# Performance work log

Hardware: AMD Instinct MI355X
Metric: run time of the kernel (lower is better)

Reference implementation:

```python
import jax, jax.numpy as jnp
import numpy as np

B, T, D = 4, 2048, 512
H, HS = 8, 64            # n_head, head_size
E, K = 8, 2              # num_experts, top_k
CAP = int(B * T * K / E * 1.0)  # expert capacity = 2048
EPS = 1e-5


def setup_inputs() -> dict:
    key = jax.random.key(0)
    ks = jax.random.split(key, 16)
    s = lambda k, shp, fan: jax.random.normal(k, shp, jnp.float32) * (fan ** -0.5)
    return {
        "x": jax.random.normal(ks[0], (B, T, D), jnp.float32),
        "ln1_g": jnp.ones((D,), jnp.float32), "ln1_b": jnp.zeros((D,), jnp.float32),
        "Wq": s(ks[1], (H, D, HS), D), "Wk": s(ks[2], (H, D, HS), D), "Wv": s(ks[3], (H, D, HS), D),
        "Wo": s(ks[4], (D, D), D), "bo": jnp.zeros((D,), jnp.float32),
        "ln2_g": jnp.ones((D,), jnp.float32), "ln2_b": jnp.zeros((D,), jnp.float32),
        "Wg": s(ks[5], (D, E), D), "bg": jnp.zeros((E,), jnp.float32),
        "Wn": s(ks[6], (D, E), D), "bn": jnp.zeros((E,), jnp.float32),
        "W1": s(ks[7], (E, D, 4 * D), D), "b1": jnp.zeros((E, 4 * D), jnp.float32),
        "W2": s(ks[8], (E, 4 * D, D), 4 * D), "b2": jnp.zeros((E, D), jnp.float32),
    }


def _ln(x, g, b):
    m = jnp.mean(x, -1, keepdims=True)
    v = jnp.var(x, -1, keepdims=True)
    return (x - m) * jax.lax.rsqrt(v + EPS) * g + b


def _attn(h, Wq, Wk, Wv, Wo, bo):
    q = jnp.einsum('btd,hde->bhte', h, Wq)
    k = jnp.einsum('btd,hde->bhte', h, Wk)
    v = jnp.einsum('btd,hde->bhte', h, Wv)
    # NOTE: source scales by C**-0.5 with C = n_embed (not head_size)
    wei = jnp.einsum('bhte,bhse->bhts', q, k) * (D ** -0.5)
    causal = jnp.tril(jnp.ones((T, T), bool))
    wei = jnp.where(causal, wei, -jnp.inf)
    wei = jax.nn.softmax(wei, axis=-1)
    out = jnp.einsum('bhts,bhse->bhte', wei, v)              # [B,H,T,HS]
    out = out.transpose(0, 2, 1, 3).reshape(B, T, D)          # concat heads
    return out @ Wo + bo


def _moe(h, Wg, bg, Wn, bn, W1, b1, W2, b2):
    logits = h @ Wg + bg
    noise_logits = h @ Wn + bn
    noise = jax.random.normal(jax.random.key(42), logits.shape, logits.dtype) * jax.nn.softplus(noise_logits)
    noisy = logits + noise
    vals, idx = jax.lax.top_k(noisy, K)                       # [B,T,K]
    # softmax over -inf-masked sparse logits == softmax over top-k values, scattered
    gates = (jax.nn.softmax(vals, -1)[..., None] * jax.nn.one_hot(idx, E, dtype=h.dtype)).sum(-2)  # [B,T,E]
    flat_x = h.reshape(-1, D)
    flat_g = gates.reshape(-1, E)
    flat_idx = idx.reshape(-1, K)
    N = flat_x.shape[0]
    mask = (flat_idx[None] == jnp.arange(E)[:, None, None]).any(-1)   # [E,N]
    rank = jnp.cumsum(mask, axis=1) - 1
    keep = mask & (rank < CAP)                                 # first CAP tokens per expert
    slot = jnp.where(keep, rank, CAP)
    tok = jnp.arange(N, dtype=jnp.int32)

    def build(s, kp):
        buf = jnp.zeros(CAP + 1, jnp.int32).at[s].set(tok)
        vb = jnp.zeros(CAP + 1, bool).at[s].set(kp)
        return buf[:CAP], vb[:CAP]

    idx_buf, valid = jax.vmap(build)(slot, keep)               # [E,CAP]
    xg = flat_x[idx_buf]                                       # [E,CAP,D]
    mid = jax.nn.relu(jnp.einsum('ecd,edf->ecf', xg, W1) + b1[:, None, :])
    out = jnp.einsum('ecf,efd->ecd', mid, W2) + b2[:, None, :]
    gate_sel = flat_g[idx_buf, jnp.arange(E)[:, None]]         # [E,CAP]
    w = out * (gate_sel * valid.astype(h.dtype))[..., None]
    upd = jnp.zeros_like(flat_x).at[idx_buf.reshape(-1)].add(w.reshape(-1, D))
    return upd.reshape(h.shape)


def reference(x, ln1_g, ln1_b, Wq, Wk, Wv, Wo, bo, ln2_g, ln2_b,
              Wg, bg, Wn, bn, W1, b1, W2, b2):
    x = x + _attn(_ln(x, ln1_g, ln1_b), Wq, Wk, Wv, Wo, bo)
    x = x + _moe(_ln(x, ln2_g, ln2_b), Wg, bg, Wn, bn, W1, b1, W2, b2)
    return x
```

## Files before the change

### kernel.cpp

```cpp
#include <hip/hip_runtime.h>
#include <math.h>

#define TSEQ 2048
#define DD   512
#define NH   8
#define HSZ  64
#define NE   8
#define NTOK 8192
#define CAPK 2048
#define FF   2048

typedef __bf16 bf16x8 __attribute__((ext_vector_type(8)));
typedef float  f32x4  __attribute__((ext_vector_type(4)));
typedef unsigned int u32;
typedef u32 u32x4 __attribute__((ext_vector_type(4)));

__device__ __forceinline__ void gload16(const void* g, void* l){
  __builtin_amdgcn_global_load_lds((const __attribute__((address_space(1))) u32*)g,
                                   (__attribute__((address_space(3))) u32*)l, 16, 0, 0);
}

__device__ __forceinline__ u32 pkbf(float a, float b){
  unsigned short ua = __builtin_bit_cast(unsigned short, (__bf16)a);
  unsigned short ub = __builtin_bit_cast(unsigned short, (__bf16)b);
  return (u32)ua | ((u32)ub << 16);
}

__device__ __forceinline__ unsigned rotl32(unsigned x, int r){ return (x<<r)|(x>>(32-r)); }

__device__ __forceinline__ void threefry2x32(unsigned c0, unsigned c1, unsigned &o0, unsigned &o1){
  const unsigned k0 = 0u, k1 = 42u;
  const unsigned k2 = k0 ^ k1 ^ 0x1BD11BDAu;
  unsigned x0 = c0 + k0, x1 = c1 + k1;
#define TFR(rot) { x0 += x1; x1 = rotl32(x1, rot); x1 ^= x0; }
  TFR(13) TFR(15) TFR(26) TFR(6)   x0 += k1; x1 += k2 + 1u;
  TFR(17) TFR(29) TFR(16) TFR(24)  x0 += k2; x1 += k0 + 2u;
  TFR(13) TFR(15) TFR(26) TFR(6)   x0 += k0; x1 += k1 + 3u;
  TFR(17) TFR(29) TFR(16) TFR(24)  x0 += k1; x1 += k2 + 4u;
  TFR(13) TFR(15) TFR(26) TFR(6)   x0 += k2; x1 += k0 + 5u;
#undef TFR
  o0 = x0; o1 = x1;
}

__device__ __forceinline__ float erfinv_f(float x){
  float w = -log1pf(-x*x);
  float p;
  if (w < 5.0f){
    w -= 2.5f;
    p = 2.81022636e-08f;
    p = fmaf(p,w, 3.43273939e-07f);
    p = fmaf(p,w,-3.5233877e-06f);
    p = fmaf(p,w,-4.39150654e-06f);
    p = fmaf(p,w, 0.00021858087f);
    p = fmaf(p,w,-0.00125372503f);
    p = fmaf(p,w,-0.00417768164f);
    p = fmaf(p,w, 0.246640727f);
    p = fmaf(p,w, 1.50140941f);
  } else {
    w = sqrtf(w) - 3.0f;
    p = -0.000200214257f;
    p = fmaf(p,w, 0.000100950558f);
    p = fmaf(p,w, 0.00134934322f);
    p = fmaf(p,w,-0.00367342844f);
    p = fmaf(p,w, 0.00573950773f);
    p = fmaf(p,w,-0.0076224613f);
    p = fmaf(p,w, 0.00943887047f);
    p = fmaf(p,w, 1.00167406f);
    p = fmaf(p,w, 2.83297682f);
  }
  return p * x;
}

__global__ __launch_bounds__(256) void ln_kernel(const float* __restrict__ x,
    const float* __restrict__ gw, const float* __restrict__ bw, float* __restrict__ o)
{
  int row  = blockIdx.x*4 + threadIdx.y;
  int lane = threadIdx.x;
  const float* xr = x + (size_t)row*DD;
  float4 a = *(const float4*)(xr + lane*4);
  float4 c = *(const float4*)(xr + 256 + lane*4);
  float s  = a.x+a.y+a.z+a.w + c.x+c.y+c.z+c.w;
  float ss = a.x*a.x+a.y*a.y+a.z*a.z+a.w*a.w + c.x*c.x+c.y*c.y+c.z*c.z+c.w*c.w;
  #pragma unroll
  for (int off = 32; off; off >>= 1){ s += __shfl_xor(s, off); ss += __shfl_xor(ss, off); }
  float m   = s * (1.0f/DD);
  float var = ss * (1.0f/DD) - m*m;
  float r   = 1.0f / sqrtf(var + 1e-5f);
  float4 g1 = *(const float4*)(gw + lane*4);
  float4 b1 = *(const float4*)(bw + lane*4);
  float4 g2 = *(const float4*)(gw + 256 + lane*4);
  float4 b2 = *(const float4*)(bw + 256 + lane*4);
  float4 o1, o2;
  o1.x=(a.x-m)*r*g1.x+b1.x; o1.y=(a.y-m)*r*g1.y+b1.y; o1.z=(a.z-m)*r*g1.z+b1.z; o1.w=(a.w-m)*r*g1.w+b1.w;
  o2.x=(c.x-m)*r*g2.x+b2.x; o2.y=(c.y-m)*r*g2.y+b2.y; o2.z=(c.z-m)*r*g2.z+b2.z; o2.w=(c.w-m)*r*g2.w+b2.w;
  float* orow = o + (size_t)row*DD;
  *(float4*)(orow + lane*4)       = o1;
  *(float4*)(orow + 256 + lane*4) = o2;
}

__global__ __launch_bounds__(256) void ln_split(const float* __restrict__ x,
    const float* __restrict__ gw, const float* __restrict__ bw,
    __bf16* __restrict__ ohi, __bf16* __restrict__ olo)
{
  int row  = blockIdx.x*4 + threadIdx.y;
  int lane = threadIdx.x;
  const float* xr = x + (size_t)row*DD;
  float4 a = *(const float4*)(xr + lane*4);
  float4 c = *(const float4*)(xr + 256 + lane*4);
  float s  = a.x+a.y+a.z+a.w + c.x+c.y+c.z+c.w;
  float ss = a.x*a.x+a.y*a.y+a.z*a.z+a.w*a.w + c.x*c.x+c.y*c.y+c.z*c.z+c.w*c.w;
  #pragma unroll
  for (int off = 32; off; off >>= 1){ s += __shfl_xor(s, off); ss += __shfl_xor(ss, off); }
  float m   = s * (1.0f/DD);
  float var = ss * (1.0f/DD) - m*m;
  float r   = 1.0f / sqrtf(var + 1e-5f);
  float4 g1 = *(const float4*)(gw + lane*4);
  float4 b1 = *(const float4*)(bw + lane*4);
  float4 g2 = *(const float4*)(gw + 256 + lane*4);
  float4 b2 = *(const float4*)(bw + 256 + lane*4);
  float f1[4], f2[4];
  f1[0]=(a.x-m)*r*g1.x+b1.x; f1[1]=(a.y-m)*r*g1.y+b1.y; f1[2]=(a.z-m)*r*g1.z+b1.z; f1[3]=(a.w-m)*r*g1.w+b1.w;
  f2[0]=(c.x-m)*r*g2.x+b2.x; f2[1]=(c.y-m)*r*g2.y+b2.y; f2[2]=(c.z-m)*r*g2.z+b2.z; f2[3]=(c.w-m)*r*g2.w+b2.w;
  __bf16 h1v[4] __attribute__((aligned(8))), l1v[4] __attribute__((aligned(8)));
  __bf16 h2v[4] __attribute__((aligned(8))), l2v[4] __attribute__((aligned(8)));
  #pragma unroll
  for (int j = 0; j < 4; ++j){
    __bf16 hb = (__bf16)f1[j]; h1v[j]=hb; l1v[j]=(__bf16)(f1[j]-(float)hb);
    __bf16 hc = (__bf16)f2[j]; h2v[j]=hc; l2v[j]=(__bf16)(f2[j]-(float)hc);
  }
  size_t base = (size_t)row*DD + lane*4;
  *(uint2*)(ohi + base)       = *(const uint2*)h1v;
  *(uint2*)(olo + base)       = *(const uint2*)l1v;
  *(uint2*)(ohi + base + 256) = *(const uint2*)h2v;
  *(uint2*)(olo + base + 256) = *(const uint2*)l2v;
}

__global__ __launch_bounds__(256) void pack_qkv_split(const float* __restrict__ Wq,
    const float* __restrict__ Wk, const float* __restrict__ Wv,
    __bf16* __restrict__ dhi, __bf16* __restrict__ dlo)
{
  __shared__ float t[64][65];
  int z = blockIdx.y;
  int kt = blockIdx.x*64;
  int sel = z >> 3, hh = z & 7;
  const float* W = (sel==0 ? Wq : (sel==1 ? Wk : Wv)) + (size_t)hh*DD*HSZ;
  int tid = threadIdx.x;
  int r = tid>>2, c0 = (tid&3)*16;
  #pragma unroll
  for (int j = 0; j < 16; j += 4){
    float4 v = *(const float4*)&W[(size_t)(kt+r)*HSZ + c0 + j];
    t[r][c0+j]=v.x; t[r][c0+j+1]=v.y; t[r][c0+j+2]=v.z; t[r][c0+j+3]=v.w;
  }
  __syncthreads();
  __bf16 hb[16] __attribute__((aligned(32)));
  __bf16 lb[16] __attribute__((aligned(32)));
  #pragma unroll
  for (int j = 0; j < 16; ++j){
    float f = t[c0+j][r];
    __bf16 h = (__bf16)f; hb[j]=h; lb[j]=(__bf16)(f-(float)h);
  }
  size_t off = (size_t)(z*64 + r)*512 + kt + c0;
  *(uint4*)(dhi+off) = ((const uint4*)hb)[0]; *(uint4*)(dhi+off+8) = ((const uint4*)hb)[1];
  *(uint4*)(dlo+off) = ((const uint4*)lb)[0]; *(uint4*)(dlo+off+8) = ((const uint4*)lb)[1];
}

__global__ __launch_bounds__(256) void transp_split(const float* __restrict__ src,
    __bf16* __restrict__ dhi, __bf16* __restrict__ dlo, int Ms, int Ns)
{
  __shared__ float t[64][65];
  int nt = blockIdx.x*64, mt = blockIdx.y*64;
  int tid = threadIdx.x;
  int r = tid>>2, c0 = (tid&3)*16;
  #pragma unroll
  for (int j = 0; j < 16; j += 4){
    float4 v = *(const float4*)&src[(size_t)(mt+r)*Ns + nt + c0 + j];
    t[r][c0+j]=v.x; t[r][c0+j+1]=v.y; t[r][c0+j+2]=v.z; t[r][c0+j+3]=v.w;
  }
  __syncthreads();
  __bf16 hb[16] __attribute__((aligned(32)));
  __bf16 lb[16] __attribute__((aligned(32)));
  #pragma unroll
  for (int j = 0; j < 16; ++j){
    float f = t[c0+j][r];
    __bf16 h = (__bf16)f; hb[j]=h; lb[j]=(__bf16)(f-(float)h);
  }
  size_t off = (size_t)(nt + r)*Ms + mt + c0;
  *(uint4*)(dhi+off) = ((const uint4*)hb)[0]; *(uint4*)(dhi+off+8) = ((const uint4*)hb)[1];
  *(uint4*)(dlo+off) = ((const uint4*)lb)[0]; *(uint4*)(dlo+off+8) = ((const uint4*)lb)[1];
}

template<int BIAS, int RES>
__global__ __launch_bounds__(256) void gemm_mfma3(
    const __bf16* __restrict__ Ahi, const __bf16* __restrict__ Alo,
    const __bf16* __restrict__ Bhi, const __bf16* __restrict__ Blo,
    const float* __restrict__ bias, const float* __restrict__ res,
    float* __restrict__ C, int M, int N, int K)
{
  __shared__ __bf16 AsH[2][4096];
  __shared__ __bf16 AsL[2][4096];
  __shared__ __bf16 BsH[2][4096];
  __shared__ __bf16 BsL[2][4096];
  int m0 = blockIdx.y*128, n0 = blockIdx.x*128;
  int tid = threadIdx.x;
  int w = tid>>6, l = tid&63;
  int wm = w>>1, wn = w&1;
  int srow = w*32 + (l>>2);
  int skb  = (l&3)<<4;
  const char* agh = (const char*)(Ahi + (size_t)(m0+srow)*K) + skb;
  const char* agl = (const char*)(Alo + (size_t)(m0+srow)*K) + skb;
  const char* bgh = (const char*)(Bhi + (size_t)(n0+srow)*K) + skb;
  const char* bgl = (const char*)(Blo + (size_t)(n0+srow)*K) + skb;
  size_t r16 = (size_t)16*K*sizeof(__bf16);

  f32x4 acc[4][4] = {};
  int rl = l & 15, kh = l >> 4;
  const __bf16* abh = &AsH[0][(wm*64 + rl)*32 + kh*8];
  const __bf16* abl = &AsL[0][(wm*64 + rl)*32 + kh*8];
  const __bf16* bbh = &BsH[0][(wn*64 + rl)*32 + kh*8];
  const __bf16* bbl = &BsL[0][(wn*64 + rl)*32 + kh*8];

  auto STAGE = [&](int bb, int kt){
    size_t o = (size_t)kt*64;
    gload16(agh+o,     &AsH[bb][w*1024]);
    gload16(agh+o+r16, &AsH[bb][w*1024+512]);
    gload16(agl+o,     &AsL[bb][w*1024]);
    gload16(agl+o+r16, &AsL[bb][w*1024+512]);
    gload16(bgh+o,     &BsH[bb][w*1024]);
    gload16(bgh+o+r16, &BsH[bb][w*1024+512]);
    gload16(bgl+o,     &BsL[bb][w*1024]);
    gload16(bgl+o+r16, &BsL[bb][w*1024+512]);
  };

  int nkt = K >> 5;
  STAGE(0, 0);
  __syncthreads();
  for (int kt = 0; kt < nkt; ++kt){
    int bb = kt & 1;
    if (kt + 1 < nkt) STAGE(bb^1, kt+1);
    bf16x8 afh[4], afl[4], bfh[4], bfl[4];
    #pragma unroll
    for (int i = 0; i < 4; ++i){
      afh[i] = *(const bf16x8*)(abh + bb*4096 + i*512);
      afl[i] = *(const bf16x8*)(abl + bb*4096 + i*512);
      bfh[i] = *(const bf16x8*)(bbh + bb*4096 + i*512);
      bfl[i] = *(const bf16x8*)(bbl + bb*4096 + i*512);
    }
    #pragma unroll
    for (int fm = 0; fm < 4; ++fm)
      #pragma unroll
      for (int fn = 0; fn < 4; ++fn){
        acc[fm][fn] = __builtin_amdgcn_mfma_f32_16x16x32_bf16(afh[fm], bfl[fn], acc[fm][fn], 0, 0, 0);
        acc[fm][fn] = __builtin_amdgcn_mfma_f32_16x16x32_bf16(afl[fm], bfh[fn], acc[fm][fn], 0, 0, 0);
        acc[fm][fn] = __builtin_amdgcn_mfma_f32_16x16x32_bf16(afh[fm], bfh[fn], acc[fm][fn], 0, 0, 0);
      }
    __syncthreads();
  }

  int ccol = l & 15, cr = (l >> 4) * 4;
  #pragma unroll
  for (int fn = 0; fn < 4; ++fn){
    int n = n0 + wn*64 + fn*16 + ccol;
    float bv = BIAS ? bias[n] : 0.0f;
    #pragma unroll
    for (int fm = 0; fm < 4; ++fm){
      int mb = m0 + wm*64 + fm*16 + cr;
      #pragma unroll
      for (int r = 0; r < 4; ++r){
        float v = acc[fm][fn][r] + bv;
        if (RES) v += res[(size_t)(mb+r)*N + n];
        C[(size_t)(mb+r)*N + n] = v;
      }
    }
  }
}

template<int STORE_BF16, int RELU>
__global__ __launch_bounds__(256) void gemm_mfma(
    const __bf16* __restrict__ A, const __bf16* __restrict__ Bt,
    const float* __restrict__ bias, void* __restrict__ Cv,
    int M, int N, int K)
{
  __shared__ __bf16 Asl[2][4096];
  __shared__ __bf16 Bsl[2][4096];
  int e = blockIdx.z;
  const __bf16* Ae = A  + (size_t)e*M*K;
  const __bf16* Be = Bt + (size_t)e*N*K;
  const float*  be = bias + (size_t)e*N;
  int m0 = blockIdx.y*128, n0 = blockIdx.x*128;
  int tid = threadIdx.x;
  int w = tid>>6, l = tid&63;
  int wm = w>>1, wn = w&1;
  int srow = w*32 + (l>>2);
  int skb  = (l&3)<<4;
  const char* ag = (const char*)(Ae + (size_t)(m0 + srow)*K) + skb;
  const char* bg = (const char*)(Be + (size_t)(n0 + srow)*K) + skb;
  size_t r16 = (size_t)16*K*sizeof(__bf16);

  f32x4 acc[4][4] = {};
  int rl = l & 15, kh = l >> 4;
  const __bf16* abase = &Asl[0][(wm*64 + rl)*32 + kh*8];
  const __bf16* bbase = &Bsl[0][(wn*64 + rl)*32 + kh*8];

  auto STAGE = [&](int bb, int kt){
    size_t o = (size_t)kt*64;
    gload16(ag+o,     &Asl[bb][w*1024]);
    gload16(ag+o+r16, &Asl[bb][w*1024+512]);
    gload16(bg+o,     &Bsl[bb][w*1024]);
    gload16(bg+o+r16, &Bsl[bb][w*1024+512]);
  };

  int nkt = K >> 5;
  STAGE(0, 0);
  __syncthreads();
  for (int kt = 0; kt < nkt; ++kt){
    int bb = kt & 1;
    if (kt + 1 < nkt) STAGE(bb^1, kt+1);
    bf16x8 af[4], bf[4];
    #pragma unroll
    for (int i = 0; i < 4; ++i){
      af[i] = *(const bf16x8*)(abase + bb*4096 + i*512);
      bf[i] = *(const bf16x8*)(bbase + bb*4096 + i*512);
    }
    #pragma unroll
    for (int fm = 0; fm < 4; ++fm)
      #pragma unroll
      for (int fn = 0; fn < 4; ++fn)
        acc[fm][fn] = __builtin_amdgcn_mfma_f32_16x16x32_bf16(af[fm], bf[fn], acc[fm][fn], 0, 0, 0);
    __syncthreads();
  }

  int ccol = l & 15, cr = (l >> 4) * 4;
  char* Ce = (char*)Cv + (size_t)e*M*N*(STORE_BF16 ? 2 : 4);
  #pragma unroll
  for (int fn = 0; fn < 4; ++fn){
    int n = n0 + wn*64 + fn*16 + ccol;
    float bv = be[n];
    #pragma unroll
    for (int fm = 0; fm < 4; ++fm){
      int mb = m0 + wm*64 + fm*16 + cr;
      #pragma unroll
      for (int r = 0; r < 4; ++r){
        float v = acc[fm][fn][r] + bv;
        if (RELU) v = fmaxf(v, 0.f);
        if (STORE_BF16) ((__bf16*)Ce)[(size_t)(mb+r)*N + n] = (__bf16)v;
        else            ((float*)Ce)[(size_t)(mb+r)*N + n] = v;
      }
    }
  }
}

__global__ __launch_bounds__(256) void transp_conv(const float* __restrict__ src,
    __bf16* __restrict__ dst, int Ms, int Ns)
{
  __shared__ __bf16 t[64][72];
  int e = blockIdx.z;
  const float* s = src + (size_t)e*Ms*Ns;
  __bf16* d = dst + (size_t)e*Ms*Ns;
  int mt = blockIdx.y*64, nt = blockIdx.x*64;
  int tid = threadIdx.x;
  int r = tid>>2, c0 = (tid&3)*16;
  #pragma unroll
  for (int j = 0; j < 16; j += 4){
    float4 v = *(const float4*)&s[(size_t)(mt+r)*Ns + nt + c0 + j];
    t[r][c0+j]   = (__bf16)v.x; t[r][c0+j+1] = (__bf16)v.y;
    t[r][c0+j+2] = (__bf16)v.z; t[r][c0+j+3] = (__bf16)v.w;
  }
  __syncthreads();
  __bf16 tmp[16] __attribute__((aligned(32)));
  #pragma unroll
  for (int j = 0; j < 16; ++j) tmp[j] = t[c0+j][r];
  uint4* dp = (uint4*)&d[(size_t)(nt+r)*Ms + mt + c0];
  dp[0] = ((const uint4*)tmp)[0];
  dp[1] = ((const uint4*)tmp)[1];
}

__global__ __launch_bounds__(256) void convert_kv(const float* __restrict__ qkv,
    __bf16* __restrict__ khi, __bf16* __restrict__ klo,
    __bf16* __restrict__ vthi, __bf16* __restrict__ vtlo)
{
  int t0 = blockIdx.x*64;
  int bh = blockIdx.y;
  int b = bh >> 3, h = bh & 7;
  int tid = threadIdx.x;
  {
    int r = tid >> 2, e0 = (tid & 3) * 16;
    const float* src = qkv + ((size_t)(b*TSEQ + t0 + r))*1536 + 512 + h*64 + e0;
    __bf16 hi[16] __attribute__((aligned(16)));
    __bf16 lo[16] __attribute__((aligned(16)));
    #pragma unroll
    for (int j = 0; j < 16; j += 4){
      float4 v = *(const float4*)(src + j);
      float f[4] = {v.x, v.y, v.z, v.w};
      #pragma unroll
      for (int q = 0; q < 4; ++q){
        __bf16 hb = (__bf16)f[q];
        hi[j+q] = hb; lo[j+q] = (__bf16)(f[q] - (float)hb);
      }
    }
    size_t off = ((size_t)(bh*TSEQ + t0 + r))*64 + e0;
    *(uint4*)(khi + off)     = ((const uint4*)hi)[0];
    *(uint4*)(khi + off + 8) = ((const uint4*)hi)[1];
    *(uint4*)(klo + off)     = ((const uint4*)lo)[0];
    *(uint4*)(klo + off + 8) = ((const uint4*)lo)[1];
  }
  {
    int key0 = (tid & 15) * 4, e0 = (tid >> 4) * 4;
    float4 v[4];
    #pragma unroll
    for (int j = 0; j < 4; ++j)
      v[j] = *(const float4*)(qkv + ((size_t)(b*TSEQ + t0 + key0 + j))*1536 + 1024 + h*64 + e0);
    float col[4][4];
    col[0][0]=v[0].x; col[0][1]=v[1].x; col[0][2]=v[2].x; col[0][3]=v[3].x;
    col[1][0]=v[0].y; col[1][1]=v[1].y; col[1][2]=v[2].y; col[1][3]=v[3].y;
    col[2][0]=v[0].z; col[2][1]=v[1].z; col[2][2]=v[2].z; col[2][3]=v[3].z;
    col[3][0]=v[0].w; col[3][1]=v[1].w; col[3][2]=v[2].w; col[3][3]=v[3].w;
    #pragma unroll
    for (int kk = 0; kk < 4; ++kk){
      __bf16 hi[4] __attribute__((aligned(8)));
      __bf16 lo[4] __attribute__((aligned(8)));
      #pragma unroll
      for (int j = 0; j < 4; ++j){
        __bf16 hb = (__bf16)col[kk][j];
        hi[j] = hb; lo[j] = (__bf16)(col[kk][j] - (float)hb);
      }
      size_t off = ((size_t)(bh*64 + e0 + kk))*TSEQ + t0 + key0;
      *(uint2*)(vthi + off) = *(const uint2*)hi;
      *(uint2*)(vtlo + off) = *(const uint2*)lo;
    }
  }
}

__global__ __launch_bounds__(512) void attn_mfma(const float* __restrict__ qkv,
    const __bf16* __restrict__ khi_g, const __bf16* __restrict__ klo_g,
    const __bf16* __restrict__ vthi_g, const __bf16* __restrict__ vtlo_g,
    __bf16* __restrict__ ahi, __bf16* __restrict__ alo)
{
  __shared__ __align__(16) char ldsbuf[65536];
  int bh = blockIdx.x;
  int qtA = blockIdx.y, qtB = 15 - qtA;
  int b = bh >> 3, h = bh & 7;
  int tid = threadIdx.x;
  int w = tid >> 6, l = tid & 63;
  int g = l >> 4, r = l & 15;
  int sA = r + 32*(g & 1);
  int sB = sA + 16;
  int ghalf = g >> 1;
  const float qsc = 0.04419417382415922f * 1.4426950408889634f;

  int qb[2]; qb[0] = qtA*128 + w*16; qb[1] = qtB*128 + (7-w)*16;
  int kdiag[2]; kdiag[0] = qb[0] >> 6; kdiag[1] = qb[1] >> 6;

  bf16x8 qhi[2][2], qlo[2][2];
  #pragma unroll
  for (int qf = 0; qf < 2; ++qf)
    #pragma unroll
    for (int ks = 0; ks < 2; ++ks){
      const float* src = qkv + ((size_t)(b*TSEQ + qb[qf] + r))*1536 + h*64 + ks*32 + g*8;
      float4 v0 = *(const float4*)src;
      float4 v1 = *(const float4*)(src + 4);
      float f[8] = {v0.x,v0.y,v0.z,v0.w,v1.x,v1.y,v1.z,v1.w};
      bf16x8 hi, lo;
      #pragma unroll
      for (int i = 0; i < 8; ++i){
        float fs = f[i] * qsc;
        __bf16 hb = (__bf16)fs;
        hi[i] = hb; lo[i] = (__bf16)(fs - (float)hb);
      }
      qhi[qf][ks] = hi; qlo[qf][ks] = lo;
    }

  f32x4 ot[4][2] = {};
  float m_r[2] = {-INFINITY, -INFINITY};
  float l_r[2] = {0.f, 0.f};

  int nkt = 2*qtB + 2;
  size_t kbase = (size_t)bh*TSEQ*64;
  size_t vbase = (size_t)bh*64*TSEQ;

  auto STAGE = [&](int buf, int kt){
    int row = tid >> 3, cc = tid & 7;
    int sw = (cc ^ (row & 7)) * 8;
    char* d = ldsbuf + buf*32768 + (w << 10);
    gload16(khi_g  + kbase + (size_t)(kt*64 + row)*64 + sw, d);
    gload16(klo_g  + kbase + (size_t)(kt*64 + row)*64 + sw, d + 8192);
    gload16(vthi_g + vbase + (size_t)row*TSEQ + kt*64 + sw,  d + 16384);
    gload16(vtlo_g + vbase + (size_t)row*TSEQ + kt*64 + sw,  d + 24576);
  };

  STAGE(0, 0);
  __syncthreads();

  for (int kt = 0; kt < nkt; ++kt){
    int buf = kt & 1;
    if (kt + 1 < nkt) STAGE(buf ^ 1, kt + 1);

    bool act[2];
    act[0] = (kt <= kdiag[0]);
    act[1] = (kt <= kdiag[1]);

    const char* K0 = ldsbuf + buf*32768;
    const char* K1 = K0 + 8192;
    const char* V0 = K0 + 16384;
    const char* V1 = K0 + 24576;

    f32x4 s[4][2] = {};
    #pragma unroll
    for (int kf = 0; kf < 4; ++kf){
      int rowk = kf*16 + r;
      int rsw = (rowk & 7) << 4;
      #pragma unroll
      for (int ks = 0; ks < 2; ++ks){
        int off = rowk*128 + ((((ks*4 + g) << 4)) ^ rsw);
        bf16x8 khf = *(const bf16x8*)(K0 + off);
        bf16x8 klf = *(const bf16x8*)(K1 + off);
        #pragma unroll
        for (int qf = 0; qf < 2; ++qf){
          if (act[qf]){
            s[kf][qf] = __builtin_amdgcn_mfma_f32_16x16x32_bf16(khf, qlo[qf][ks], s[kf][qf], 0,0,0);
            s[kf][qf] = __builtin_amdgcn_mfma_f32_16x16x32_bf16(klf, qhi[qf][ks], s[kf][qf], 0,0,0);
            s[kf][qf] = __builtin_amdgcn_mfma_f32_16x16x32_bf16(khf, qhi[qf][ks], s[kf][qf], 0,0,0);
          }
        }
      }
    }

    u32 phi[4][2][2], plo[4][2][2];
    #pragma unroll
    for (int qf = 0; qf < 2; ++qf){
      if (act[qf]){
        int q = qb[qf] + r;
        float p[4][4];
        float mx = -INFINITY;
        if (kt == kdiag[qf]){
          #pragma unroll
          for (int kf = 0; kf < 4; ++kf)
            #pragma unroll
            for (int e = 0; e < 4; ++e){
              int key = kt*64 + kf*16 + g*4 + e;
              float sv = (key <= q) ? s[kf][qf][e] : -INFINITY;
              p[kf][e] = sv;
              mx = fmaxf(mx, sv);
            }
        } else {
          #pragma unroll
          for (int kf = 0; kf < 4; ++kf)
            #pragma unroll
            for (int e = 0; e < 4; ++e){
              float sv = s[kf][qf][e];
              p[kf][e] = sv;
              mx = fmaxf(mx, sv);
            }
        }
        mx = fmaxf(mx, __shfl_xor(mx, 16));
        mx = fmaxf(mx, __shfl_xor(mx, 32));
        if (__any(mx > m_r[qf])){
          float mn = fmaxf(m_r[qf], mx);
          float fj = exp2f(m_r[qf] - mn);
          m_r[qf] = mn;
          l_r[qf] *= fj;
          #pragma unroll
          for (int ef = 0; ef < 4; ++ef)
            #pragma unroll
            for (int e = 0; e < 4; ++e)
              ot[ef][qf][e] *= fj;
        }
        float ts = 0.f;
        #pragma unroll
        for (int kf = 0; kf < 4; ++kf)
          #pragma unroll
          for (int e = 0; e < 4; ++e){
            float pv = exp2f(p[kf][e] - m_r[qf]);
            p[kf][e] = pv; ts += pv;
          }
        ts += __shfl_xor(ts, 16); ts += __shfl_xor(ts, 32);
        l_r[qf] += ts;
        #pragma unroll
        for (int kf = 0; kf < 4; ++kf){
          __bf16 h0=(__bf16)p[kf][0], h1=(__bf16)p[kf][1], h2=(__bf16)p[kf][2], h3=(__bf16)p[kf][3];
          phi[kf][qf][0] = pkbf(p[kf][0], p[kf][1]);
          phi[kf][qf][1] = pkbf(p[kf][2], p[kf][3]);
          plo[kf][qf][0] = pkbf(p[kf][0]-(float)h0, p[kf][1]-(float)h1);
          plo[kf][qf][1] = pkbf(p[kf][2]-(float)h2, p[kf][3]-(float)h3);
        }
      }
    }

    #pragma unroll
    for (int ks = 0; ks < 2; ++ks){
      u32x4 pbh[2], pbl[2];
      #pragma unroll
      for (int qf = 0; qf < 2; ++qf){
        if (act[qf]){
          #pragma unroll
          for (int p2 = 0; p2 < 2; ++p2){
            u32 hA0 = (u32)__shfl((int)phi[2*ks  ][qf][p2], sA);
            u32 hA1 = (u32)__shfl((int)phi[2*ks+1][qf][p2], sA);
            u32 hB0 = (u32)__shfl((int)phi[2*ks  ][qf][p2], sB);
            u32 hB1 = (u32)__shfl((int)phi[2*ks+1][qf][p2], sB);
            pbh[qf][p2]   = ghalf ? hA1 : hA0;
            pbh[qf][2+p2] = ghalf ? hB1 : hB0;
            u32 lA0 = (u32)__shfl((int)plo[2*ks  ][qf][p2], sA);
            u32 lA1 = (u32)__shfl((int)plo[2*ks+1][qf][p2], sA);
            u32 lB0 = (u32)__shfl((int)plo[2*ks  ][qf][p2], sB);
            u32 lB1 = (u32)__shfl((int)plo[2*ks+1][qf][p2], sB);
            pbl[qf][p2]   = ghalf ? lA1 : lA0;
            pbl[qf][2+p2] = ghalf ? lB1 : lB0;
          }
        }
      }
      #pragma unroll
      for (int ef = 0; ef < 4; ++ef){
        int rowv = ef*16 + r;
        int off = rowv*128 + ((((ks*4 + g) << 4)) ^ ((rowv & 7) << 4));
        bf16x8 vhf = *(const bf16x8*)(V0 + off);
        bf16x8 vlf = *(const bf16x8*)(V1 + off);
        #pragma unroll
        for (int qf = 0; qf < 2; ++qf){
          if (act[qf]){
            bf16x8 ph = __builtin_bit_cast(bf16x8, pbh[qf]);
            bf16x8 pl = __builtin_bit_cast(bf16x8, pbl[qf]);
            ot[ef][qf] = __builtin_amdgcn_mfma_f32_16x16x32_bf16(vhf, pl, ot[ef][qf], 0,0,0);
            ot[ef][qf] = __builtin_amdgcn_mfma_f32_16x16x32_bf16(vlf, ph, ot[ef][qf], 0,0,0);
            ot[ef][qf] = __builtin_amdgcn_mfma_f32_16x16x32_bf16(vhf, ph, ot[ef][qf], 0,0,0);
          }
        }
      }
    }
    __syncthreads();
  }

  float* Osh = (float*)ldsbuf;
  #pragma unroll
  for (int qf = 0; qf < 2; ++qf){
    float inv = 1.0f / l_r[qf];
    int qloc = (qf ? (7-w) : w)*16 + r;
    #pragma unroll
    for (int ef = 0; ef < 4; ++ef)
      #pragma unroll
      for (int e = 0; e < 4; ++e)
        Osh[qloc*68 + ef*16 + g*4 + e] = ot[ef][qf][e] * inv;
    __syncthreads();
    {
      int qt = qf ? qtB : qtA;
      int q = tid >> 2, e0 = (tid & 3)*16;
      const float* srow = Osh + q*68 + e0;
      size_t base = ((size_t)(b*TSEQ + qt*128 + q))*DD + h*64 + e0;
      #pragma unroll
      for (int j = 0; j < 4; ++j){
        float4 v = *(const float4*)(srow + j*4);
        float f[4] = {v.x, v.y, v.z, v.w};
        __bf16 hb[4] __attribute__((aligned(8)));
        __bf16 lb[4] __attribute__((aligned(8)));
        #pragma unroll
        for (int q2 = 0; q2 < 4; ++q2){
          __bf16 h2b = (__bf16)f[q2];
          hb[q2] = h2b; lb[q2] = (__bf16)(f[q2] - (float)h2b);
        }
        *(uint2*)(ahi + base + j*4) = *(const uint2*)hb;
        *(uint2*)(alo + base + j*4) = *(const uint2*)lb;
      }
    }
    __syncthreads();
  }
}

__global__ __launch_bounds__(256) void router_kernel(const float* __restrict__ h2,
    const float* __restrict__ Wg, const float* __restrict__ bg,
    const float* __restrict__ Wn, const float* __restrict__ bn,
    int* __restrict__ idx0, int* __restrict__ idx1,
    float* __restrict__ g0, float* __restrict__ g1)
{
  int wid = threadIdx.x >> 6, lane = threadIdx.x & 63;
  int tok = blockIdx.x*4 + wid;
  const float* xr = h2 + (size_t)tok*DD;
  float ag[8] = {0,0,0,0,0,0,0,0}, an[8] = {0,0,0,0,0,0,0,0};
  for (int d = lane; d < DD; d += 64){
    float xv = xr[d];
    const float* wg = Wg + d*8;
    const float* wn = Wn + d*8;
    #pragma unroll
    for (int e = 0; e < 8; ++e){ ag[e] = fmaf(xv, wg[e], ag[e]); an[e] = fmaf(xv, wn[e], an[e]); }
  }
  #pragma unroll
  for (int off = 32; off; off >>= 1){
    #pragma unroll
    for (int e = 0; e < 8; ++e){ ag[e] += __shfl_xor(ag[e], off); an[e] += __shfl_xor(an[e], off); }
  }
  __shared__ float ns[4][8];
  if (lane < 8){
    int e = lane;
    float lg = ag[e] + bg[e];
    float nl = an[e] + bn[e];
    float sp = fmaxf(nl, 0.f) + log1pf(expf(-fabsf(nl)));
    unsigned i = (unsigned)(tok*8 + e);
    unsigned r0b, r1b;
    threefry2x32(0u, i, r0b, r1b);
    unsigned bits = r0b ^ r1b;
    float f = __uint_as_float((bits >> 9) | 0x3f800000u) - 1.0f;
    float u = fmaf(f, 2.0f, -0.99999994f);
    u = fmaxf(u, -0.99999994f);
    float z = 1.41421356f * erfinv_f(u);
    ns[wid][e] = lg + z*sp;
  }
  __syncthreads();
  if (lane == 0){
    float v0 = -INFINITY; int i0 = 0;
    #pragma unroll
    for (int e = 0; e < 8; ++e){ float v = ns[wid][e]; if (v > v0){ v0 = v; i0 = e; } }
    float v1 = -INFINITY; int i1 = 0;
    #pragma unroll
    for (int e = 0; e < 8; ++e){ if (e != i0){ float v = ns[wid][e]; if (v > v1){ v1 = v; i1 = e; } } }
    float dexp = expf(v1 - v0);
    float ssum = 1.0f + dexp;
    idx0[tok] = i0; idx1[tok] = i1;
    g0[tok] = 1.0f/ssum; g1[tok] = dexp/ssum;
  }
}

__global__ __launch_bounds__(256) void route_scan(const int* __restrict__ idx0,
    const int* __restrict__ idx1, int* __restrict__ idx_buf, int* __restrict__ tok_slot)
{
  int e = blockIdx.x, tid = threadIdx.x;
  for (int i = tid; i < CAPK; i += 256) idx_buf[e*CAPK + i] = 0;
  __syncthreads();
  int base = tid * 32;
  int cnt = 0;
  for (int j = 0; j < 32; ++j){ int t = base + j; cnt += (idx0[t]==e || idx1[t]==e) ? 1 : 0; }
  __shared__ int ps[256];
  ps[tid] = cnt; __syncthreads();
  for (int off = 1; off < 256; off <<= 1){
    int add = (tid >= off) ? ps[tid - off] : 0;
    __syncthreads();
    ps[tid] += add;
    __syncthreads();
  }
  int slot = ps[tid] - cnt;
  for (int j = 0; j < 32; ++j){
    int t = base + j;
    int k = (idx0[t]==e) ? 0 : ((idx1[t]==e) ? 1 : -1);
    if (k >= 0){
      if (slot < CAPK){ idx_buf[e*CAPK + slot] = t; tok_slot[t*2 + k] = slot; }
      else            { tok_slot[t*2 + k] = -1; }
      slot++;
    }
  }
}

__global__ __launch_bounds__(128) void gather_bf16(const float* __restrict__ h2,
    const int* __restrict__ idx_buf, __bf16* __restrict__ xg)
{
  int ec = blockIdx.x;
  int tok = idx_buf[ec];
  float4 v = ((const float4*)(h2 + (size_t)tok*DD))[threadIdx.x];
  __bf16 o[4] __attribute__((aligned(8)));
  o[0]=(__bf16)v.x; o[1]=(__bf16)v.y; o[2]=(__bf16)v.z; o[3]=(__bf16)v.w;
  ((uint2*)(xg + (size_t)ec*DD))[threadIdx.x] = *(const uint2*)o;
}

__global__ __launch_bounds__(128) void combine_kernel(const float* __restrict__ x1,
    const __bf16* __restrict__ eout, const int* __restrict__ idx0, const int* __restrict__ idx1,
    const float* __restrict__ g0, const float* __restrict__ g1,
    const int* __restrict__ tok_slot, float* __restrict__ outp)
{
  int n = blockIdx.x, t = threadIdx.x;
  float4 acc = *(const float4*)(x1 + (size_t)n*DD + t*4);
  #pragma unroll
  for (int k = 0; k < 2; ++k){
    int s = tok_slot[n*2 + k];
    if (s >= 0){
      int e  = (k==0) ? idx0[n] : idx1[n];
      float g = (k==0) ? g0[n] : g1[n];
      __bf16 vb[4] __attribute__((aligned(8)));
      *(uint2*)vb = *(const uint2*)(eout + ((size_t)(e*CAPK + s))*DD + t*4);
      acc.x = fmaf(g, (float)vb[0], acc.x); acc.y = fmaf(g, (float)vb[1], acc.y);
      acc.z = fmaf(g, (float)vb[2], acc.z); acc.w = fmaf(g, (float)vb[3], acc.w);
    }
  }
  *(float4*)(outp + (size_t)n*DD + t*4) = acc;
}

extern "C" void kernel_launch(void* const* d_in, const int* in_sizes, int n_in,
                              void* d_out, int out_size, void* d_ws, size_t ws_size,
                              hipStream_t stream)
{
  const float* x    = (const float*)d_in[0];
  const float* ln1g = (const float*)d_in[1];
  const float* ln1b = (const float*)d_in[2];
  const float* Wq   = (const float*)d_in[3];
  const float* Wk   = (const float*)d_in[4];
  const float* Wv   = (const float*)d_in[5];
  const float* Wo   = (const float*)d_in[6];
  const float* bo   = (const float*)d_in[7];
  const float* ln2g = (const float*)d_in[8];
  const float* ln2b = (const float*)d_in[9];
  const float* Wg   = (const float*)d_in[10];
  const float* bg   = (const float*)d_in[11];
  const float* Wn   = (const float*)d_in[12];
  const float* bn   = (const float*)d_in[13];
  const float* W1   = (const float*)d_in[14];
  const float* b1   = (const float*)d_in[15];
  const float* W2   = (const float*)d_in[16];
  const float* b2   = (const float*)d_in[17];
  float* out = (float*)d_out;
  char* ws = (char*)d_ws;
  const size_t MB = 1u << 20;

  __bf16* h1hi   = (__bf16*)(ws);
  __bf16* h1lo   = (__bf16*)(ws + 8*MB);
  __bf16* attnhi = (__bf16*)(ws);
  __bf16* attnlo = (__bf16*)(ws + 8*MB);
  float*  h2     = (float*)(ws);
  float*  qkv    = (float*)(ws + 16*MB);
  __bf16* W1T    = (__bf16*)(ws + 16*MB);
  __bf16* W2T    = (__bf16*)(ws + 32*MB);
  __bf16* xg     = (__bf16*)(ws + 48*MB);
  float*  x1     = (float*)(ws + 64*MB);
  __bf16* Khi    = (__bf16*)(ws + 80*MB);
  __bf16* Klo    = (__bf16*)(ws + 88*MB);
  __bf16* Vthi   = (__bf16*)(ws + 96*MB);
  __bf16* Vtlo   = (__bf16*)(ws + 104*MB);
  __bf16* Bqh    = (__bf16*)(ws + 80*MB);
  __bf16* Bql    = (__bf16*)(ws + 82*MB);
  __bf16* eoutb  = (__bf16*)(ws + 80*MB);
  __bf16* mid    = (__bf16*)(ws + 112*MB);
  __bf16* WoTh   = (__bf16*)(ws + 144*MB);
  __bf16* WoTl   = (__bf16*)(ws + 144*MB + 512*1024);
  char*   smallp = ws + 145*MB;
  int*   idx0     = (int*)smallp;
  int*   idx1     = idx0 + NTOK;
  float* g0       = (float*)(idx1 + NTOK);
  float* g1       = g0 + NTOK;
  int*   tok_slot = (int*)(g1 + NTOK);
  int*   idx_buf  = tok_slot + NTOK*2;

  ln_split<<<dim3(NTOK/4), dim3(64,4), 0, stream>>>(x, ln1g, ln1b, h1hi, h1lo);
  pack_qkv_split<<<dim3(8,24), 256, 0, stream>>>(Wq, Wk, Wv, Bqh, Bql);
  transp_split<<<dim3(8,8), 256, 0, stream>>>(Wo, WoTh, WoTl, DD, DD);
  gemm_mfma3<0,0><<<dim3(12,64), 256, 0, stream>>>(h1hi, h1lo, Bqh, Bql, nullptr, nullptr, qkv, NTOK, 1536, DD);
  convert_kv<<<dim3(TSEQ/64, 32), 256, 0, stream>>>(qkv, Khi, Klo, Vthi, Vtlo);
  attn_mfma<<<dim3(32, 8), 512, 0, stream>>>(qkv, Khi, Klo, Vthi, Vtlo, attnhi, attnlo);
  gemm_mfma3<1,1><<<dim3(4,64), 256, 0, stream>>>(attnhi, attnlo, WoTh, WoTl, bo, x, x1, NTOK, DD, DD);
  ln_kernel<<<dim3(NTOK/4), dim3(64,4), 0, stream>>>(x1, ln2g, ln2b, h2);
  transp_conv<<<dim3(32,8,NE), 256, 0, stream>>>(W1, W1T, DD, FF);
  transp_conv<<<dim3(8,32,NE), 256, 0, stream>>>(W2, W2T, FF, DD);
  router_kernel<<<dim3(NTOK/4), 256, 0, stream>>>(h2, Wg, bg, Wn, bn, idx0, idx1, g0, g1);
  route_scan<<<dim3(NE), 256, 0, stream>>>(idx0, idx1, idx_buf, tok_slot);
  gather_bf16<<<dim3(NE*CAPK), 128, 0, stream>>>(h2, idx_buf, xg);
  for (int gg = 0; gg < 2; ++gg){
    gemm_mfma<1,1><<<dim3(FF/128, CAPK/128, 4), 256, 0, stream>>>(
        xg + (size_t)gg*4*CAPK*DD, W1T + (size_t)gg*4*DD*FF, b1 + (size_t)gg*4*FF,
        mid, CAPK, FF, DD);
    gemm_mfma<1,0><<<dim3(DD/128, CAPK/128, 4), 256, 0, stream>>>(
        mid, W2T + (size_t)gg*4*FF*DD, b2 + (size_t)gg*4*DD,
        eoutb + (size_t)gg*4*CAPK*DD, CAPK, DD, FF);
  }
  combine_kernel<<<dim3(NTOK), 128, 0, stream>>>(x1, eoutb, idx0, idx1, g0, g1, tok_slot, out);
}
```

Before: 436.5 us.

## Fuse LN2 into router, gather tokens inside expert GEMM, flatten grid

LayerNorm2 is folded into the router kernel, which now writes a bf16 copy of the normalized activations and computes the routing logits from registers. The separate gather kernel is removed, and the first expert GEMM reads token rows directly through idx_buf while staging A tiles. The expert GEMMs also move to a flattened 1D grid with the expert index in the low bits, so blocks of different experts interleave. Together this removes two launches and the fp32 h2 and xg round trips through memory, at the cost of irregular, non-contiguous A loads in the GEMM.

```diff
diff --git a/kernel.cpp b/kernel.cpp
--- a/kernel.cpp
+++ b/kernel.cpp
@@ -71,33 +71,6 @@
   return p * x;
 }
 
-__global__ __launch_bounds__(256) void ln_kernel(const float* __restrict__ x,
-    const float* __restrict__ gw, const float* __restrict__ bw, float* __restrict__ o)
-{
-  int row  = blockIdx.x*4 + threadIdx.y;
-  int lane = threadIdx.x;
-  const float* xr = x + (size_t)row*DD;
-  float4 a = *(const float4*)(xr + lane*4);
-  float4 c = *(const float4*)(xr + 256 + lane*4);
-  float s  = a.x+a.y+a.z+a.w + c.x+c.y+c.z+c.w;
-  float ss = a.x*a.x+a.y*a.y+a.z*a.z+a.w*a.w + c.x*c.x+c.y*c.y+c.z*c.z+c.w*c.w;
-  #pragma unroll
-  for (int off = 32; off; off >>= 1){ s += __shfl_xor(s, off); ss += __shfl_xor(ss, off); }
-  float m   = s * (1.0f/DD);
-  float var = ss * (1.0f/DD) - m*m;
-  float r   = 1.0f / sqrtf(var + 1e-5f);
-  float4 g1 = *(const float4*)(gw + lane*4);
-  float4 b1 = *(const float4*)(bw + lane*4);
-  float4 g2 = *(const float4*)(gw + 256 + lane*4);
-  float4 b2 = *(const float4*)(bw + 256 + lane*4);
-  float4 o1, o2;
-  o1.x=(a.x-m)*r*g1.x+b1.x; o1.y=(a.y-m)*r*g1.y+b1.y; o1.z=(a.z-m)*r*g1.z+b1.z; o1.w=(a.w-m)*r*g1.w+b1.w;
-  o2.x=(c.x-m)*r*g2.x+b2.x; o2.y=(c.y-m)*r*g2.y+b2.y; o2.z=(c.z-m)*r*g2.z+b2.z; o2.w=(c.w-m)*r*g2.w+b2.w;
-  float* orow = o + (size_t)row*DD;
-  *(float4*)(orow + lane*4)       = o1;
-  *(float4*)(orow + 256 + lane*4) = o2;
-}
-
 __global__ __launch_bounds__(256) void ln_split(const float* __restrict__ x,
     const float* __restrict__ gw, const float* __restrict__ bw,
     __bf16* __restrict__ ohi, __bf16* __restrict__ olo)
@@ -274,39 +247,54 @@
   }
 }
 
-template<int STORE_BF16, int RELU>
+template<int STORE_BF16, int RELU, int GATHER, int LOGN>
 __global__ __launch_bounds__(256) void gemm_mfma(
     const __bf16* __restrict__ A, const __bf16* __restrict__ Bt,
     const float* __restrict__ bias, void* __restrict__ Cv,
-    int M, int N, int K)
+    const int* __restrict__ idxb, int M, int N, int K)
 {
   __shared__ __bf16 Asl[2][4096];
   __shared__ __bf16 Bsl[2][4096];
-  int e = blockIdx.z;
-  const __bf16* Ae = A  + (size_t)e*M*K;
+  int flat = blockIdx.x;
+  int e = flat & 3;
+  int tile = flat >> 2;
+  int n0 = (tile & ((1<<LOGN)-1)) * 128;
+  int m0 = (tile >> LOGN) * 128;
   const __bf16* Be = Bt + (size_t)e*N*K;
   const float*  be = bias + (size_t)e*N;
-  int m0 = blockIdx.y*128, n0 = blockIdx.x*128;
   int tid = threadIdx.x;
   int w = tid>>6, l = tid&63;
   int wm = w>>1, wn = w&1;
   int srow = w*32 + (l>>2);
   int skb  = (l&3)<<4;
-  const char* ag = (const char*)(Ae + (size_t)(m0 + srow)*K) + skb;
+  const char* ag;
+  if (GATHER){
+    int tok = idxb[e*CAPK + m0 + srow];
+    ag = (const char*)(A + (size_t)tok*K) + skb;
+  } else {
+    ag = (const char*)(A + (size_t)e*M*K + (size_t)(m0 + srow)*K) + skb;
+  }
   const char* bg = (const char*)(Be + (size_t)(n0 + srow)*K) + skb;
-  size_t r16 = (size_t)16*K*sizeof(__bf16);
+  size_t r16;
+  if (GATHER){
+    int tok2 = idxb[e*CAPK + m0 + srow + 16];
+    r16 = (size_t)((const char*)(A + (size_t)tok2*K) + skb - ag);
+  } else {
+    r16 = (size_t)16*K*sizeof(__bf16);
+  }
 
   f32x4 acc[4][4] = {};
   int rl = l & 15, kh = l >> 4;
   const __bf16* abase = &Asl[0][(wm*64 + rl)*32 + kh*8];
   const __bf16* bbase = &Bsl[0][(wn*64 + rl)*32 + kh*8];
 
+  size_t br16 = (size_t)16*K*sizeof(__bf16);
   auto STAGE = [&](int bb, int kt){
     size_t o = (size_t)kt*64;
-    gload16(ag+o,     &Asl[bb][w*1024]);
-    gload16(ag+o+r16, &Asl[bb][w*1024+512]);
-    gload16(bg+o,     &Bsl[bb][w*1024]);
-    gload16(bg+o+r16, &Bsl[bb][w*1024+512]);
+    gload16(ag+o,      &Asl[bb][w*1024]);
+    gload16(ag+o+r16,  &Asl[bb][w*1024+512]);
+    gload16(bg+o,      &Bsl[bb][w*1024]);
+    gload16(bg+o+br16, &Bsl[bb][w*1024+512]);
   };
 
   int nkt = K >> 5;
@@ -664,22 +652,55 @@
   }
 }
 
-__global__ __launch_bounds__(256) void router_kernel(const float* __restrict__ h2,
+__global__ __launch_bounds__(256) void routerln_kernel(const float* __restrict__ x1,
+    const float* __restrict__ gw, const float* __restrict__ bw,
     const float* __restrict__ Wg, const float* __restrict__ bg,
     const float* __restrict__ Wn, const float* __restrict__ bn,
+    __bf16* __restrict__ h2b,
     int* __restrict__ idx0, int* __restrict__ idx1,
     float* __restrict__ g0, float* __restrict__ g1)
 {
   int wid = threadIdx.x >> 6, lane = threadIdx.x & 63;
   int tok = blockIdx.x*4 + wid;
-  const float* xr = h2 + (size_t)tok*DD;
+  const float* xr = x1 + (size_t)tok*DD;
+  float4 a = *(const float4*)(xr + lane*4);
+  float4 c = *(const float4*)(xr + 256 + lane*4);
+  float s  = a.x+a.y+a.z+a.w + c.x+c.y+c.z+c.w;
+  float ss = a.x*a.x+a.y*a.y+a.z*a.z+a.w*a.w + c.x*c.x+c.y*c.y+c.z*c.z+c.w*c.w;
+  #pragma unroll
+  for (int off = 32; off; off >>= 1){ s += __shfl_xor(s, off); ss += __shfl_xor(ss, off); }
+  float m   = s * (1.0f/DD);
+  float var = ss * (1.0f/DD) - m*m;
+  float rr  = 1.0f / sqrtf(var + 1e-5f);
+  float4 g1v = *(const float4*)(gw + lane*4);
+  float4 b1v = *(const float4*)(bw + lane*4);
+  float4 g2v = *(const float4*)(gw + 256 + lane*4);
+  float4 b2v = *(const float4*)(bw + 256 + lane*4);
+  float f1[4], f2[4];
+  f1[0]=(a.x-m)*rr*g1v.x+b1v.x; f1[1]=(a.y-m)*rr*g1v.y+b1v.y; f1[2]=(a.z-m)*rr*g1v.z+b1v.z; f1[3]=(a.w-m)*rr*g1v.w+b1v.w;
+  f2[0]=(c.x-m)*rr*g2v.x+b2v.x; f2[1]=(c.y-m)*rr*g2v.y+b2v.y; f2[2]=(c.z-m)*rr*g2v.z+b2v.z; f2[3]=(c.w-m)*rr*g2v.w+b2v.w;
+  {
+    __bf16 h1v[4] __attribute__((aligned(8)));
+    __bf16 h2v[4] __attribute__((aligned(8)));
+    #pragma unroll
+    for (int j = 0; j < 4; ++j){ h1v[j] = (__bf16)f1[j]; h2v[j] = (__bf16)f2[j]; }
+    size_t base = (size_t)tok*DD + lane*4;
+    *(uint2*)(h2b + base)       = *(const uint2*)h1v;
+    *(uint2*)(h2b + base + 256) = *(const uint2*)h2v;
+  }
   float ag[8] = {0,0,0,0,0,0,0,0}, an[8] = {0,0,0,0,0,0,0,0};
-  for (int d = lane; d < DD; d += 64){
-    float xv = xr[d];
-    const float* wg = Wg + d*8;
-    const float* wn = Wn + d*8;
-    #pragma unroll
-    for (int e = 0; e < 8; ++e){ ag[e] = fmaf(xv, wg[e], ag[e]); an[e] = fmaf(xv, wn[e], an[e]); }
+  int d1 = lane*4, d2 = 256 + lane*4;
+  #pragma unroll
+  for (int j = 0; j < 4; ++j){
+    const float* wg1 = Wg + (size_t)(d1+j)*8;
+    const float* wn1 = Wn + (size_t)(d1+j)*8;
+    const float* wg2 = Wg + (size_t)(d2+j)*8;
+    const float* wn2 = Wn + (size_t)(d2+j)*8;
+    #pragma unroll
+    for (int e = 0; e < 8; ++e){
+      ag[e] = fmaf(f1[j], wg1[e], ag[e]); an[e] = fmaf(f1[j], wn1[e], an[e]);
+      ag[e] = fmaf(f2[j], wg2[e], ag[e]); an[e] = fmaf(f2[j], wn2[e], an[e]);
+    }
   }
   #pragma unroll
   for (int off = 32; off; off >>= 1){
@@ -744,17 +765,6 @@
       slot++;
     }
   }
-}
-
-__global__ __launch_bounds__(128) void gather_bf16(const float* __restrict__ h2,
-    const int* __restrict__ idx_buf, __bf16* __restrict__ xg)
-{
-  int ec = blockIdx.x;
-  int tok = idx_buf[ec];
-  float4 v = ((const float4*)(h2 + (size_t)tok*DD))[threadIdx.x];
-  __bf16 o[4] __attribute__((aligned(8)));
-  o[0]=(__bf16)v.x; o[1]=(__bf16)v.y; o[2]=(__bf16)v.z; o[3]=(__bf16)v.w;
-  ((uint2*)(xg + (size_t)ec*DD))[threadIdx.x] = *(const uint2*)o;
 }
 
 __global__ __launch_bounds__(128) void combine_kernel(const float* __restrict__ x1,
@@ -809,11 +819,10 @@
   __bf16* h1lo   = (__bf16*)(ws + 8*MB);
   __bf16* attnhi = (__bf16*)(ws);
   __bf16* attnlo = (__bf16*)(ws + 8*MB);
-  float*  h2     = (float*)(ws);
+  __bf16* h2b    = (__bf16*)(ws);
   float*  qkv    = (float*)(ws + 16*MB);
   __bf16* W1T    = (__bf16*)(ws + 16*MB);
   __bf16* W2T    = (__bf16*)(ws + 32*MB);
-  __bf16* xg     = (__bf16*)(ws + 48*MB);
   float*  x1     = (float*)(ws + 64*MB);
   __bf16* Khi    = (__bf16*)(ws + 80*MB);
   __bf16* Klo    = (__bf16*)(ws + 88*MB);
@@ -840,19 +849,18 @@
   convert_kv<<<dim3(TSEQ/64, 32), 256, 0, stream>>>(qkv, Khi, Klo, Vthi, Vtlo);
   attn_mfma<<<dim3(32, 8), 512, 0, stream>>>(qkv, Khi, Klo, Vthi, Vtlo, attnhi, attnlo);
   gemm_mfma3<1,1><<<dim3(4,64), 256, 0, stream>>>(attnhi, attnlo, WoTh, WoTl, bo, x, x1, NTOK, DD, DD);
-  ln_kernel<<<dim3(NTOK/4), dim3(64,4), 0, stream>>>(x1, ln2g, ln2b, h2);
+  routerln_kernel<<<dim3(NTOK/4), 256, 0, stream>>>(x1, ln2g, ln2b, Wg, bg, Wn, bn,
+      h2b, idx0, idx1, g0, g1);
   transp_conv<<<dim3(32,8,NE), 256, 0, stream>>>(W1, W1T, DD, FF);
   transp_conv<<<dim3(8,32,NE), 256, 0, stream>>>(W2, W2T, FF, DD);
-  router_kernel<<<dim3(NTOK/4), 256, 0, stream>>>(h2, Wg, bg, Wn, bn, idx0, idx1, g0, g1);
   route_scan<<<dim3(NE), 256, 0, stream>>>(idx0, idx1, idx_buf, tok_slot);
-  gather_bf16<<<dim3(NE*CAPK), 128, 0, stream>>>(h2, idx_buf, xg);
   for (int gg = 0; gg < 2; ++gg){
-    gemm_mfma<1,1><<<dim3(FF/128, CAPK/128, 4), 256, 0, stream>>>(
-        xg + (size_t)gg*4*CAPK*DD, W1T + (size_t)gg*4*DD*FF, b1 + (size_t)gg*4*FF,
-        mid, CAPK, FF, DD);
-    gemm_mfma<1,0><<<dim3(DD/128, CAPK/128, 4), 256, 0, stream>>>(
+    gemm_mfma<1,1,1,4><<<dim3(4*16*16), 256, 0, stream>>>(
+        h2b, W1T + (size_t)gg*4*DD*FF, b1 + (size_t)gg*4*FF,
+        mid, idx_buf + (size_t)gg*4*CAPK, CAPK, FF, DD);
+    gemm_mfma<1,0,0,2><<<dim3(4*4*16), 256, 0, stream>>>(
         mid, W2T + (size_t)gg*4*FF*DD, b2 + (size_t)gg*4*DD,
-        eoutb + (size_t)gg*4*CAPK*DD, CAPK, DD, FF);
+        eoutb + (size_t)gg*4*CAPK*DD, nullptr, CAPK, DD, FF);
   }
   combine_kernel<<<dim3(NTOK), 128, 0, stream>>>(x1, eoutb, idx0, idx1, g0, g1, tok_slot, out);
 }
```

After: 433.6 us. About the same (-0.7%).
